# Kernel tuning notes

Measured on AMD Instinct MI355X. Metric: run time of the kernel, lower is better.

The kernel has to match this reference:

```python
import jax, jax.numpy as jnp
import numpy as np

D_MODEL = 512
D_FF = 2048
NUM_EXPERTS = 8
TOP_K = 2


def setup_inputs() -> dict:
    key = jax.random.key(0)
    ks = jax.random.split(key, 6)
    scale = 0.02
    x = jax.random.normal(ks[0], (4, 8192, D_MODEL), dtype=jnp.float32)
    gate_w = jax.random.normal(ks[1], (D_MODEL, NUM_EXPERTS), dtype=jnp.float32) * scale
    w1 = jax.random.normal(ks[2], (NUM_EXPERTS, D_MODEL, D_FF), dtype=jnp.float32) * scale
    b1 = jnp.zeros((NUM_EXPERTS, D_FF), dtype=jnp.float32)
    w2 = jax.random.normal(ks[3], (NUM_EXPERTS, D_FF, D_MODEL), dtype=jnp.float32) * scale
    b2 = jnp.zeros((NUM_EXPERTS, D_MODEL), dtype=jnp.float32)
    return {"x": x, "gate_w": gate_w, "w1": w1, "b1": b1, "w2": w2, "b2": b2}


def reference(x, gate_w, w1, b1, w2, b2):
    B, S, D = x.shape
    xt = x.reshape(-1, D)                                  # [T, D]
    logits = xt @ gate_w                                   # [T, E]
    probs = jax.nn.softmax(logits, axis=-1)
    top_p, top_i = jax.lax.top_k(probs, TOP_K)             # [T, K]
    top_p = top_p / jnp.sum(top_p, axis=-1, keepdims=True)
    # per-token combine weight for each expert: [T, E]
    w_te = jnp.sum(jax.nn.one_hot(top_i, NUM_EXPERTS, dtype=xt.dtype) * top_p[..., None], axis=1)
    out = jnp.zeros_like(xt)
    for e in range(NUM_EXPERTS):  # small fixed loop over experts
        h = jax.nn.gelu(xt @ w1[e] + b1[e], approximate=False)  # [T, d_ff]
        y = h @ w2[e] + b2[e]                                   # [T, D]
        out = out + w_te[:, e:e + 1] * y
    return out.reshape(B, S, D)
```

## Files before the change

### kernel.cpp

```cpp
#include <hip/hip_runtime.h>
#include <math.h>

#define T_TOK 32768
#define DM 512
#define DFF 2048
#define NE 8
#define MAXTILES 528

typedef __attribute__((ext_vector_type(8))) short short8;
typedef __attribute__((ext_vector_type(4))) float f32x4;

__device__ __forceinline__ unsigned int f2bf1(float f) {
  union { float f; unsigned int u; } x; x.f = f;
  return (x.u + 0x7fffu + ((x.u >> 16) & 1u)) >> 16;
}

#define GLOAD(src, dst) \
  __builtin_amdgcn_global_load_lds((const __attribute__((address_space(1))) unsigned int*)(src), \
                                   (__attribute__((address_space(3))) unsigned int*)(dst), 16, 0, 0)

__global__ void tcvt_kernel(const float* __restrict__ src, unsigned short* __restrict__ dst,
                            int R, int C) {
  __shared__ float tile[32][33];
  int e = blockIdx.z;
  const float* s = src + (size_t)e * R * C;
  unsigned short* d = dst + (size_t)e * R * C;
  int c0 = blockIdx.x * 32, r0 = blockIdx.y * 32;
  int tx = threadIdx.x, ty = threadIdx.y;
#pragma unroll
  for (int i = 0; i < 4; ++i)
    tile[ty + i * 8][tx] = s[(size_t)(r0 + ty + i * 8) * C + c0 + tx];
  __syncthreads();
#pragma unroll
  for (int i = 0; i < 4; ++i)
    d[(size_t)(c0 + ty + i * 8) * R + r0 + tx] = (unsigned short)f2bf1(tile[tx][ty + i * 8]);
}

__global__ __launch_bounds__(1024) void gate_kernel(
    const float* __restrict__ x, const float* __restrict__ gw,
    int* __restrict__ cnt, int* __restrict__ tok, float* __restrict__ wgt,
    unsigned int* __restrict__ xb) {
  __shared__ int lcnt[NE];
  __shared__ int lbase[NE];
  __shared__ int wslot[16][2];
  __shared__ int winfo[16][2];
  __shared__ float wval[16][2];
  int tid = threadIdx.x;
  int wid = tid >> 6, lane = tid & 63;
  int t = blockIdx.x * 16 + wid;
  if (tid < NE) lcnt[tid] = 0;
  __syncthreads();

  float acc[NE];
#pragma unroll
  for (int e = 0; e < NE; ++e) acc[e] = 0.f;
  const float* xr = x + (size_t)t * DM;
  unsigned int* xbr = xb + (size_t)t * (DM / 2);
#pragma unroll
  for (int j = 0; j < 4; ++j) {
    int d0 = j * 128 + lane * 2;
    float2 xv = *(const float2*)(xr + d0);
    const float* g0 = gw + d0 * NE;
#pragma unroll
    for (int e = 0; e < NE; ++e) acc[e] += xv.x * g0[e] + xv.y * g0[NE + e];
    xbr[j * 64 + lane] = f2bf1(xv.x) | (f2bf1(xv.y) << 16);
  }
#pragma unroll
  for (int off = 32; off >= 1; off >>= 1) {
#pragma unroll
    for (int e = 0; e < NE; ++e) acc[e] += __shfl_xor(acc[e], off);
  }
  if (lane == 0) {
    int e0 = 0; float l0 = acc[0];
#pragma unroll
    for (int e = 1; e < NE; ++e) if (acc[e] > l0) { l0 = acc[e]; e0 = e; }
    int e1 = (e0 == 0) ? 1 : 0; float l1 = acc[e1];
#pragma unroll
    for (int e = 0; e < NE; ++e) if (e != e0 && acc[e] > l1) { l1 = acc[e]; e1 = e; }
    float w0 = 1.f / (1.f + expf(l1 - l0));
    winfo[wid][0] = e0; winfo[wid][1] = e1;
    wval[wid][0] = w0;  wval[wid][1] = 1.f - w0;
    wslot[wid][0] = atomicAdd(&lcnt[e0], 1);
    wslot[wid][1] = atomicAdd(&lcnt[e1], 1);
  }
  __syncthreads();
  if (tid < NE) lbase[tid] = atomicAdd(&cnt[tid * 64], lcnt[tid]);
  __syncthreads();
  if (lane == 0) {
    int e0 = winfo[wid][0], e1 = winfo[wid][1];
    int p0 = lbase[e0] + wslot[wid][0];
    int p1 = lbase[e1] + wslot[wid][1];
    tok[e0 * T_TOK + p0] = t; wgt[e0 * T_TOK + p0] = wval[wid][0];
    tok[e1 * T_TOK + p1] = t; wgt[e1 * T_TOK + p1] = wval[wid][1];
  }
}

__global__ void plan_kernel(const int* __restrict__ cnt, int* __restrict__ tile_base) {
  if (threadIdx.x == 0 && blockIdx.x == 0) {
    int tb = 0;
    for (int e = 0; e < NE; ++e) { tile_base[e] = tb; tb += (cnt[e * 64] + 127) >> 7; }
    tile_base[NE] = tb;
  }
}

__global__ __launch_bounds__(256) void gemm1_kernel(
    const unsigned int* __restrict__ xb, const unsigned short* __restrict__ w1t,
    const float* __restrict__ b1, const int* __restrict__ cnt,
    const int* __restrict__ tok, const int* __restrict__ tile_base,
    unsigned short* __restrict__ H, int tile_lo) {
  int bid = (int)blockIdx.x;
  int nt = bid & 15;
  int gt = tile_lo + (bid >> 4);
  if (gt >= tile_base[NE]) return;
  int e = 0;
#pragma unroll
  for (int k = 0; k < NE - 1; ++k) e += (gt >= tile_base[k + 1]) ? 1 : 0;
  int tloc = gt - tile_base[e];
  int ce = cnt[e * 64];
  int m0 = tloc * 128;
  int n0 = nt * 128;

  __shared__ unsigned short As[2][128 * 32];
  __shared__ unsigned short Bs[2][128 * 32];

  int tid = (int)threadIdx.x;
  int lane = tid & 63;
  int wid = tid >> 6;
  int wm = wid & 1, wn = wid >> 1;
  int fl = lane & 15, q = lane >> 4;
  int sxy = ((q ^ ((fl >> 1) & 3)) << 4);

  const int* tokg = tok + e * T_TOK;
  int r0 = tid >> 2, r1 = 64 + (tid >> 2);
  int sl = tid & 3;
  int ss0 = sl ^ ((r0 >> 1) & 3);
  int ss1 = sl ^ ((r1 >> 1) & 3);
  int t0 = tokg[min(m0 + r0, ce - 1)];
  int t1 = tokg[min(m0 + r1, ce - 1)];
  const char* asrc0 = (const char*)xb + (size_t)t0 * 1024 + ss0 * 16;
  const char* asrc1 = (const char*)xb + (size_t)t1 * 1024 + ss1 * 16;
  const char* bsrc0 = (const char*)w1t + ((size_t)e * DFF + n0 + r0) * 1024 + ss0 * 16;
  const char* bsrc1 = (const char*)w1t + ((size_t)e * DFF + n0 + r1) * 1024 + ss1 * 16;

  int aoff[4], boff[4];
#pragma unroll
  for (int i = 0; i < 4; ++i) {
    aoff[i] = (wm * 64 + i * 16 + fl) * 64 + sxy;
    boff[i] = (wn * 64 + i * 16 + fl) * 64 + sxy;
  }

  f32x4 acc[4][4];
#pragma unroll
  for (int a = 0; a < 4; ++a)
#pragma unroll
    for (int b = 0; b < 4; ++b) acc[a][b] = (f32x4){0.f, 0.f, 0.f, 0.f};

#define STAGE1(AB, BB, ko) do { \
    GLOAD(asrc0 + (ko), (char*)(AB) + tid * 16);        \
    GLOAD(asrc1 + (ko), (char*)(AB) + 4096 + tid * 16); \
    GLOAD(bsrc0 + (ko), (char*)(BB) + tid * 16);        \
    GLOAD(bsrc1 + (ko), (char*)(BB) + 4096 + tid * 16); } while (0)

#define COMP1(AB, BB) do { \
    short8 a[4], b[4]; \
    _Pragma("unroll") for (int i = 0; i < 4; ++i) { \
      a[i] = *(const short8*)((const char*)(AB) + aoff[i]); \
      b[i] = *(const short8*)((const char*)(BB) + boff[i]); } \
    _Pragma("unroll") for (int mf = 0; mf < 4; ++mf) \
    _Pragma("unroll") for (int nf = 0; nf < 4; ++nf) \
      acc[mf][nf] = __builtin_amdgcn_mfma_f32_16x16x32_bf16(a[mf], b[nf], acc[mf][nf], 0, 0, 0); \
  } while (0)

  STAGE1(As[0], Bs[0], 0);
  __syncthreads();
  for (int t = 0; t < 16; t += 2) {
    STAGE1(As[1], Bs[1], (size_t)(t + 1) * 64);
    COMP1(As[0], Bs[0]);
    __syncthreads();
    if (t + 2 < 16) STAGE1(As[0], Bs[0], (size_t)(t + 2) * 64);
    COMP1(As[1], Bs[1]);
    __syncthreads();
  }
#undef STAGE1
#undef COMP1

  size_t hrow0 = (size_t)(gt - tile_lo) * 128;
#pragma unroll
  for (int nf = 0; nf < 4; ++nf) {
    float bias = b1[e * DFF + n0 + wn * 64 + nf * 16 + fl];
    int col = n0 + wn * 64 + nf * 16 + fl;
#pragma unroll
    for (int mf = 0; mf < 4; ++mf)
#pragma unroll
      for (int j = 0; j < 4; ++j) {
        int row = wm * 64 + mf * 16 + q * 4 + j;
        float v = acc[mf][nf][j] + bias;
        v = 0.5f * v * (1.f + erff(v * 0.70710678118654752f));
        H[(hrow0 + row) * DFF + col] = (unsigned short)f2bf1(v);
      }
  }
}

__global__ __launch_bounds__(256) void gemm2_kernel(
    const unsigned short* __restrict__ H, const unsigned short* __restrict__ w2t,
    const float* __restrict__ b2, const int* __restrict__ cnt,
    const int* __restrict__ tok, const float* __restrict__ wgt,
    const int* __restrict__ tile_base, float* __restrict__ out, int tile_lo) {
  int bid = (int)blockIdx.x;
  int nt = bid & 3;
  int gt = tile_lo + (bid >> 2);
  if (gt >= tile_base[NE]) return;
  int e = 0;
#pragma unroll
  for (int k = 0; k < NE - 1; ++k) e += (gt >= tile_base[k + 1]) ? 1 : 0;
  int tloc = gt - tile_base[e];
  int ce = cnt[e * 64];
  int m0 = tloc * 128;
  int n0 = nt * 128;

  __shared__ unsigned short As[2][128 * 32];
  __shared__ unsigned short Bs[2][128 * 32];

  int tid = (int)threadIdx.x;
  int lane = tid & 63;
  int wid = tid >> 6;
  int wm = wid & 1, wn = wid >> 1;
  int fl = lane & 15, q = lane >> 4;
  int sxy = ((q ^ ((fl >> 1) & 3)) << 4);

  int r0 = tid >> 2, r1 = 64 + (tid >> 2);
  int sl = tid & 3;
  int ss0 = sl ^ ((r0 >> 1) & 3);
  int ss1 = sl ^ ((r1 >> 1) & 3);
  size_t hrow0 = (size_t)(gt - tile_lo) * 128;
  const char* asrc0 = (const char*)H + (hrow0 + r0) * 4096 + ss0 * 16;
  const char* asrc1 = (const char*)H + (hrow0 + r1) * 4096 + ss1 * 16;
  const char* bsrc0 = (const char*)w2t + ((size_t)e * DM + n0 + r0) * 4096 + ss0 * 16;
  const char* bsrc1 = (const char*)w2t + ((size_t)e * DM + n0 + r1) * 4096 + ss1 * 16;

  int aoff[4], boff[4];
#pragma unroll
  for (int i = 0; i < 4; ++i) {
    aoff[i] = (wm * 64 + i * 16 + fl) * 64 + sxy;
    boff[i] = (wn * 64 + i * 16 + fl) * 64 + sxy;
  }

  f32x4 acc[4][4];
#pragma unroll
  for (int a = 0; a < 4; ++a)
#pragma unroll
    for (int b = 0; b < 4; ++b) acc[a][b] = (f32x4){0.f, 0.f, 0.f, 0.f};

#define STAGE2(AB, BB, ko) do { \
    GLOAD(asrc0 + (ko), (char*)(AB) + tid * 16);        \
    GLOAD(asrc1 + (ko), (char*)(AB) + 4096 + tid * 16); \
    GLOAD(bsrc0 + (ko), (char*)(BB) + tid * 16);        \
    GLOAD(bsrc1 + (ko), (char*)(BB) + 4096 + tid * 16); } while (0)

#define COMP2(AB, BB) do { \
    short8 a[4], b[4]; \
    _Pragma("unroll") for (int i = 0; i < 4; ++i) { \
      a[i] = *(const short8*)((const char*)(AB) + aoff[i]); \
      b[i] = *(const short8*)((const char*)(BB) + boff[i]); } \
    _Pragma("unroll") for (int mf = 0; mf < 4; ++mf) \
    _Pragma("unroll") for (int nf = 0; nf < 4; ++nf) \
      acc[mf][nf] = __builtin_amdgcn_mfma_f32_16x16x32_bf16(a[mf], b[nf], acc[mf][nf], 0, 0, 0); \
  } while (0)

  STAGE2(As[0], Bs[0], 0);
  __syncthreads();
  for (int t = 0; t < 64; t += 2) {
    STAGE2(As[1], Bs[1], (size_t)(t + 1) * 64);
    COMP2(As[0], Bs[0]);
    __syncthreads();
    if (t + 2 < 64) STAGE2(As[0], Bs[0], (size_t)(t + 2) * 64);
    COMP2(As[1], Bs[1]);
    __syncthreads();
  }
#undef STAGE2
#undef COMP2

  const int* tokg = tok + e * T_TOK;
  const float* wgtg = wgt + e * T_TOK;
  float bias2[4];
#pragma unroll
  for (int nf = 0; nf < 4; ++nf) bias2[nf] = b2[e * DM + n0 + wn * 64 + nf * 16 + fl];
#pragma unroll
  for (int mf = 0; mf < 4; ++mf)
#pragma unroll
    for (int j = 0; j < 4; ++j) {
      int row = wm * 64 + mf * 16 + q * 4 + j;
      int slot = m0 + row;
      if (slot < ce) {
        int tk = tokg[slot];
        float w = wgtg[slot];
        float* orow = out + (size_t)tk * DM + n0 + wn * 64;
#pragma unroll
        for (int nf = 0; nf < 4; ++nf)
          atomicAdd(orow + nf * 16 + fl, w * (acc[mf][nf][j] + bias2[nf]));
      }
    }
}

extern "C" void kernel_launch(void* const* d_in, const int* in_sizes, int n_in,
                              void* d_out, int out_size, void* d_ws, size_t ws_size,
                              hipStream_t stream) {
  (void)in_sizes; (void)n_in; (void)out_size;
  const float* x  = (const float*)d_in[0];
  const float* gw = (const float*)d_in[1];
  const float* w1 = (const float*)d_in[2];
  const float* b1 = (const float*)d_in[3];
  const float* w2 = (const float*)d_in[4];
  const float* b2 = (const float*)d_in[5];
  float* out = (float*)d_out;

  char* ws = (char*)d_ws;
  size_t off = 0;
  auto alloc = [&](size_t sz) { char* p = ws + off; off += (sz + 255) & ~(size_t)255; return p; };
  int*   cnt = (int*)alloc(NE * 64 * 4);
  int*   tok = (int*)alloc((size_t)NE * T_TOK * 4);
  float* wgt = (float*)alloc((size_t)NE * T_TOK * 4);
  int*   tile_base = (int*)alloc((NE + 1) * 4);
  unsigned int* xb = (unsigned int*)alloc((size_t)T_TOK * (DM / 2) * 4);
  unsigned short* w1t = (unsigned short*)alloc((size_t)NE * DFF * DM * 2);
  unsigned short* w2t = (unsigned short*)alloc((size_t)NE * DM * DFF * 2);

  size_t avail = (ws_size > off) ? (ws_size - off) : 0;
  int TPC = MAXTILES, NC = 1;
  while (NC < 32 && (size_t)TPC * 128 * DFF * 2 > avail) {
    NC *= 2; TPC = (MAXTILES + NC - 1) / NC;
  }
  unsigned short* H = (unsigned short*)alloc((size_t)TPC * 128 * DFF * 2);

  hipMemsetAsync(cnt, 0, NE * 64 * 4, stream);
  hipMemsetAsync(out, 0, (size_t)T_TOK * DM * 4, stream);

  tcvt_kernel<<<dim3(DFF / 32, DM / 32, NE), dim3(32, 8), 0, stream>>>(w1, w1t, DM, DFF);
  tcvt_kernel<<<dim3(DM / 32, DFF / 32, NE), dim3(32, 8), 0, stream>>>(w2, w2t, DFF, DM);
  gate_kernel<<<T_TOK / 16, 1024, 0, stream>>>(x, gw, cnt, tok, wgt, xb);
  plan_kernel<<<1, 64, 0, stream>>>(cnt, tile_base);

  for (int c = 0; c < NC; ++c) {
    int lo = c * TPC;
    if (lo >= MAXTILES) break;
    gemm1_kernel<<<TPC * 16, 256, 0, stream>>>(xb, w1t, b1, cnt, tok, tile_base, H, lo);
    gemm2_kernel<<<TPC * 4, 256, 0, stream>>>(H, w2t, b2, cnt, tok, wgt, tile_base, out, lo);
  }
}
```

Baseline: 685.9 us.

## Deepen GEMM LDS pipeline to five-stage ring with explicit vmcnt waits

```diff
diff --git a/kernel.cpp b/kernel.cpp
--- a/kernel.cpp
+++ b/kernel.cpp
@@ -18,6 +18,8 @@
 #define GLOAD(src, dst) \
   __builtin_amdgcn_global_load_lds((const __attribute__((address_space(1))) unsigned int*)(src), \
                                    (__attribute__((address_space(3))) unsigned int*)(dst), 16, 0, 0)
+#define WAITVM(N) asm volatile("s_waitcnt vmcnt(" #N ")" ::: "memory")
+#define BARRIER() asm volatile("s_barrier" ::: "memory")
 
 __global__ void tcvt_kernel(const float* __restrict__ src, unsigned short* __restrict__ dst,
                             int R, int C) {
@@ -120,8 +122,7 @@
   int m0 = tloc * 128;
   int n0 = nt * 128;
 
-  __shared__ unsigned short As[2][128 * 32];
-  __shared__ unsigned short Bs[2][128 * 32];
+  __shared__ char Lds[5 * 16384];
 
   int tid = (int)threadIdx.x;
   int lane = tid & 63;
@@ -146,7 +147,7 @@
 #pragma unroll
   for (int i = 0; i < 4; ++i) {
     aoff[i] = (wm * 64 + i * 16 + fl) * 64 + sxy;
-    boff[i] = (wn * 64 + i * 16 + fl) * 64 + sxy;
+    boff[i] = 8192 + (wn * 64 + i * 16 + fl) * 64 + sxy;
   }
 
   f32x4 acc[4][4];
@@ -155,32 +156,35 @@
 #pragma unroll
     for (int b = 0; b < 4; ++b) acc[a][b] = (f32x4){0.f, 0.f, 0.f, 0.f};
 
-#define STAGE1(AB, BB, ko) do { \
-    GLOAD(asrc0 + (ko), (char*)(AB) + tid * 16);        \
-    GLOAD(asrc1 + (ko), (char*)(AB) + 4096 + tid * 16); \
-    GLOAD(bsrc0 + (ko), (char*)(BB) + tid * 16);        \
-    GLOAD(bsrc1 + (ko), (char*)(BB) + 4096 + tid * 16); } while (0)
-
-#define COMP1(AB, BB) do { \
+#define STAGE1(bi, ti) do { \
+    char* base_ = Lds + (bi) * 16384; size_t ko_ = (size_t)(ti) * 64; \
+    GLOAD(asrc0 + ko_, base_ + tid * 16);        \
+    GLOAD(asrc1 + ko_, base_ + 4096 + tid * 16); \
+    GLOAD(bsrc0 + ko_, base_ + 8192 + tid * 16); \
+    GLOAD(bsrc1 + ko_, base_ + 12288 + tid * 16); } while (0)
+
+#define COMP1(bi) do { \
+    const char* base_ = Lds + (bi) * 16384; \
     short8 a[4], b[4]; \
     _Pragma("unroll") for (int i = 0; i < 4; ++i) { \
-      a[i] = *(const short8*)((const char*)(AB) + aoff[i]); \
-      b[i] = *(const short8*)((const char*)(BB) + boff[i]); } \
+      a[i] = *(const short8*)(base_ + aoff[i]); \
+      b[i] = *(const short8*)(base_ + boff[i]); } \
     _Pragma("unroll") for (int mf = 0; mf < 4; ++mf) \
     _Pragma("unroll") for (int nf = 0; nf < 4; ++nf) \
       acc[mf][nf] = __builtin_amdgcn_mfma_f32_16x16x32_bf16(a[mf], b[nf], acc[mf][nf], 0, 0, 0); \
   } while (0)
 
-  STAGE1(As[0], Bs[0], 0);
-  __syncthreads();
-  for (int t = 0; t < 16; t += 2) {
-    STAGE1(As[1], Bs[1], (size_t)(t + 1) * 64);
-    COMP1(As[0], Bs[0]);
-    __syncthreads();
-    if (t + 2 < 16) STAGE1(As[0], Bs[0], (size_t)(t + 2) * 64);
-    COMP1(As[1], Bs[1]);
-    __syncthreads();
-  }
+  STAGE1(0, 0); STAGE1(1, 1); STAGE1(2, 2); STAGE1(3, 3);
+  int c0 = 0, c1 = 4;
+  for (int t = 0; t < 13; ++t) {
+    WAITVM(12);
+    BARRIER();
+    if (t + 4 < 16) { STAGE1(c1, t + 4); c1 = (c1 == 4) ? 0 : c1 + 1; }
+    COMP1(c0); c0 = (c0 == 4) ? 0 : c0 + 1;
+  }
+  WAITVM(8);  BARRIER(); COMP1(c0); c0 = (c0 == 4) ? 0 : c0 + 1;
+  WAITVM(4);  BARRIER(); COMP1(c0); c0 = (c0 == 4) ? 0 : c0 + 1;
+  WAITVM(0);  BARRIER(); COMP1(c0);
 #undef STAGE1
 #undef COMP1
 
@@ -218,8 +222,7 @@
   int m0 = tloc * 128;
   int n0 = nt * 128;
 
-  __shared__ unsigned short As[2][128 * 32];
-  __shared__ unsigned short Bs[2][128 * 32];
+  __shared__ char Lds[5 * 16384];
 
   int tid = (int)threadIdx.x;
   int lane = tid & 63;
@@ -242,7 +245,7 @@
 #pragma unroll
   for (int i = 0; i < 4; ++i) {
     aoff[i] = (wm * 64 + i * 16 + fl) * 64 + sxy;
-    boff[i] = (wn * 64 + i * 16 + fl) * 64 + sxy;
+    boff[i] = 8192 + (wn * 64 + i * 16 + fl) * 64 + sxy;
   }
 
   f32x4 acc[4][4];
@@ -251,32 +254,35 @@
 #pragma unroll
     for (int b = 0; b < 4; ++b) acc[a][b] = (f32x4){0.f, 0.f, 0.f, 0.f};
 
-#define STAGE2(AB, BB, ko) do { \
-    GLOAD(asrc0 + (ko), (char*)(AB) + tid * 16);        \
-    GLOAD(asrc1 + (ko), (char*)(AB) + 4096 + tid * 16); \
-    GLOAD(bsrc0 + (ko), (char*)(BB) + tid * 16);        \
-    GLOAD(bsrc1 + (ko), (char*)(BB) + 4096 + tid * 16); } while (0)
-
-#define COMP2(AB, BB) do { \
+#define STAGE2(bi, ti) do { \
+    char* base_ = Lds + (bi) * 16384; size_t ko_ = (size_t)(ti) * 64; \
+    GLOAD(asrc0 + ko_, base_ + tid * 16);        \
+    GLOAD(asrc1 + ko_, base_ + 4096 + tid * 16); \
+    GLOAD(bsrc0 + ko_, base_ + 8192 + tid * 16); \
+    GLOAD(bsrc1 + ko_, base_ + 12288 + tid * 16); } while (0)
+
+#define COMP2(bi) do { \
+    const char* base_ = Lds + (bi) * 16384; \
     short8 a[4], b[4]; \
     _Pragma("unroll") for (int i = 0; i < 4; ++i) { \
-      a[i] = *(const short8*)((const char*)(AB) + aoff[i]); \
-      b[i] = *(const short8*)((const char*)(BB) + boff[i]); } \
+      a[i] = *(const short8*)(base_ + aoff[i]); \
+      b[i] = *(const short8*)(base_ + boff[i]); } \
     _Pragma("unroll") for (int mf = 0; mf < 4; ++mf) \
     _Pragma("unroll") for (int nf = 0; nf < 4; ++nf) \
       acc[mf][nf] = __builtin_amdgcn_mfma_f32_16x16x32_bf16(a[mf], b[nf], acc[mf][nf], 0, 0, 0); \
   } while (0)
 
-  STAGE2(As[0], Bs[0], 0);
-  __syncthreads();
-  for (int t = 0; t < 64; t += 2) {
-    STAGE2(As[1], Bs[1], (size_t)(t + 1) * 64);
-    COMP2(As[0], Bs[0]);
-    __syncthreads();
-    if (t + 2 < 64) STAGE2(As[0], Bs[0], (size_t)(t + 2) * 64);
-    COMP2(As[1], Bs[1]);
-    __syncthreads();
-  }
+  STAGE2(0, 0); STAGE2(1, 1); STAGE2(2, 2); STAGE2(3, 3);
+  int c0 = 0, c1 = 4;
+  for (int t = 0; t < 61; ++t) {
+    WAITVM(12);
+    BARRIER();
+    if (t + 4 < 64) { STAGE2(c1, t + 4); c1 = (c1 == 4) ? 0 : c1 + 1; }
+    COMP2(c0); c0 = (c0 == 4) ? 0 : c0 + 1;
+  }
+  WAITVM(8);  BARRIER(); COMP2(c0); c0 = (c0 == 4) ? 0 : c0 + 1;
+  WAITVM(4);  BARRIER(); COMP2(c0); c0 = (c0 == 4) ? 0 : c0 + 1;
+  WAITVM(0);  BARRIER(); COMP2(c0);
 #undef STAGE2
 #undef COMP2
 
```

Result: faster. 628.4 us (-8.4%).
